# Performance work log

Hardware: AMD Instinct MI355X
Metric: run time of the kernel (lower is better)

The kernel has to match this reference:

```python
import math
import jax, jax.numpy as jnp
import numpy as np

B, N_COLS, CHANNELS, NUM_HEADS = 512, 128, 512, 8
D_HEAD = CHANNELS // NUM_HEADS


def setup_inputs() -> dict:
    key = jax.random.key(0)
    ks = jax.random.split(key, 9)
    s = 1.0 / math.sqrt(CHANNELS)
    x = jax.random.normal(ks[0], (B, N_COLS, CHANNELS), dtype=jnp.float32)
    Wq = jax.random.uniform(ks[1], (CHANNELS, CHANNELS), jnp.float32, -s, s)
    bq = jax.random.uniform(ks[2], (CHANNELS,), jnp.float32, -s, s)
    Wk = jax.random.uniform(ks[3], (CHANNELS, CHANNELS), jnp.float32, -s, s)
    bk = jax.random.uniform(ks[4], (CHANNELS,), jnp.float32, -s, s)
    Wv = jax.random.uniform(ks[5], (CHANNELS, CHANNELS), jnp.float32, -s, s)
    bv = jax.random.uniform(ks[6], (CHANNELS,), jnp.float32, -s, s)
    Wo = jax.random.uniform(ks[7], (CHANNELS, CHANNELS), jnp.float32, -s, s)
    bo = jax.random.uniform(ks[8], (CHANNELS,), jnp.float32, -s, s)
    return {"x": x, "Wq": Wq, "bq": bq, "Wk": Wk, "bk": bk,
            "Wv": Wv, "bv": bv, "Wo": Wo, "bo": bo}


def reference(x, Wq, bq, Wk, bk, Wv, bv, Wo, bo):
    b, n, c = x.shape
    h, d = NUM_HEADS, D_HEAD

    def split_heads(t):  # [b, n, c] -> [b, h, n, d]
        return t.reshape(b, n, h, d).transpose(0, 2, 1, 3)

    Q = split_heads(x @ Wq + bq)
    K = split_heads(x @ Wk + bk)
    V = split_heads(x @ Wv + bv)

    # raw scores [b, h, q, k]
    scores = jnp.einsum('bhqd,bhkd->bhqk', Q, K)
    # causal mask over columns; note: mask added BEFORE scaling by sqrt(d)
    causal = jnp.tril(jnp.ones((n, n), dtype=jnp.float32))
    mask = (1.0 - causal) * -100000.0
    attn = jax.nn.softmax((scores + mask) / math.sqrt(d), axis=-1)
    out = jnp.einsum('bhqk,bhkd->bhqd', attn, V)
    out = out.transpose(0, 2, 1, 3).reshape(b, n, c)
    return out @ Wo + bo
```

## Files before the change

kernel.cpp:

```cpp
#include <hip/hip_runtime.h>

typedef _Float16 f16;
typedef _Float16 half8 __attribute__((ext_vector_type(8)));
typedef _Float16 half4 __attribute__((ext_vector_type(4)));
typedef float f32x4 __attribute__((ext_vector_type(4)));

#define B_SZ 512
#define NQ   128
#define CH   512
#define NH   8
#define DH   64
#define MTOK (B_SZ*NQ)
#define KD   512

#define MFMA16(a,b,c) __builtin_amdgcn_mfma_f32_16x16x32_f16((a),(b),(c),0,0,0)

#define GLDS16(g,l) __builtin_amdgcn_global_load_lds( \
    (__attribute__((address_space(1))) void*)(g), \
    (__attribute__((address_space(3))) void*)(l), 16, 0, 0)

__global__ __launch_bounds__(256) void k_prep(
    const float* __restrict__ x,
    const float* __restrict__ Wq, const float* __restrict__ Wk,
    const float* __restrict__ Wv, const float* __restrict__ Wo,
    f16* __restrict__ xb, f16* __restrict__ wt) {
  const int bid = blockIdx.x;
  if (bid < 512) {
    for (int e = threadIdx.x; e < 2048; e += 256) {
      const int n = bid * 4 + (e >> 9);
      const int k = e & 511;
      const float* W = (n < 512) ? Wq : (n < 1024) ? Wk : (n < 1536) ? Wv : Wo;
      wt[n * 512 + k] = (f16)W[k * 512 + (n & 511)];
    }
  } else {
    const int n8 = MTOK * KD / 8;
    int i = (bid - 512) * 256 + threadIdx.x;
    const int stride = 2048 * 256;
    for (; i < n8; i += stride) {
      f32x4 a = ((const f32x4*)x)[2 * i];
      f32x4 b = ((const f32x4*)x)[2 * i + 1];
      half8 h;
      h[0] = (f16)a[0]; h[1] = (f16)a[1]; h[2] = (f16)a[2]; h[3] = (f16)a[3];
      h[4] = (f16)b[0]; h[5] = (f16)b[1]; h[6] = (f16)b[2]; h[7] = (f16)b[3];
      ((half8*)xb)[i] = h;
    }
  }
}

__device__ __forceinline__ void gemm128_bk64(
    const f16* __restrict__ gA,
    const f16* __restrict__ gB,
    f16* la, f16* lb, f32x4 (&acc)[4][4]) {
  const int tid = threadIdx.x;
  const int w = tid >> 6, lane = tid & 63;
  const int ln = lane & 15, g = lane >> 4;
  const int wr = w >> 1, wc = w & 1;

  const int ldst = w * 512;
  const int roA0 = (wr * 64 + ln) * 64;
  const int roB0 = (wc * 64 + ln) * 64;
  const int sx0 = ((0 * 4 + g) ^ (ln & 7)) * 8;
  const int sx1 = ((1 * 4 + g) ^ (ln & 7)) * 8;

#pragma unroll 1
  for (int kt = 0; kt < 8; ++kt) {
    const int k0 = kt * 64;
#pragma unroll
    for (int i = 0; i < 4; ++i) {
      GLDS16(gA + i * 32 * KD + k0, la + i * 2048 + ldst);
      GLDS16(gB + i * 32 * KD + k0, lb + i * 2048 + ldst);
    }
    __syncthreads();
    half8 af[4], bf[4];
#pragma unroll
    for (int ks = 0; ks < 2; ++ks) {
      const int sx = ks ? sx1 : sx0;
#pragma unroll
      for (int m = 0; m < 4; ++m)
        af[m] = *(const half8*)(la + roA0 + m * 1024 + sx);
#pragma unroll
      for (int n = 0; n < 4; ++n)
        bf[n] = *(const half8*)(lb + roB0 + n * 1024 + sx);
      __builtin_amdgcn_s_setprio(1);
#pragma unroll
      for (int m = 0; m < 4; ++m)
#pragma unroll
        for (int n = 0; n < 4; ++n)
          acc[m][n] = MFMA16(af[m], bf[n], acc[m][n]);
      __builtin_amdgcn_s_setprio(0);
    }
    __syncthreads();
  }
}

__device__ __forceinline__ int stage_src_off() {
  const int lane = threadIdx.x & 63, w = threadIdx.x >> 6;
  return (w * 8 + (lane >> 3)) * KD + (((lane & 7) ^ (lane >> 3)) << 3);
}

__global__ __launch_bounds__(256, 4) void k_qkv(
    const f16* __restrict__ A, const f16* __restrict__ Bw,
    const float* __restrict__ bq, const float* __restrict__ bk,
    const float* __restrict__ bv,
    f16* __restrict__ qb, f16* __restrict__ kb, f16* __restrict__ vb) {
  __shared__ f16 la[128 * 64];
  __shared__ f16 lb[128 * 64];
  const int tid = threadIdx.x;
  const int w = tid >> 6, lane = tid & 63;
  const int ln = lane & 15, g = lane >> 4;
  const int wr = w >> 1, wc = w & 1;
  const int s = blockIdx.x >> 3;
  const int ml = s / 12;
  const int ntile = s - ml * 12;
  const int mtile = (blockIdx.x & 7) * 64 + ml;

  const int so = stage_src_off();
  const f16* gA = A + mtile * 128 * KD + so;
  const f16* gB = Bw + ntile * 128 * KD + so;

  f32x4 acc[4][4] = {};
  gemm128_bk64(gA, gB, la, lb, acc);

  const int b = mtile;
  const int colbase = ntile * 128 + wc * 64;
#pragma unroll
  for (int m = 0; m < 4; ++m) {
    const int nn0 = wr * 64 + m * 16 + g * 4;
#pragma unroll
    for (int n = 0; n < 4; ++n) {
      const int col = colbase + n * 16 + ln;
      const int which = col >> 9;
      const int c = col & 511;
      const int h = c >> 6, d = c & 63;
      const float bias = (which == 0) ? bq[c] : (which == 1) ? bk[c] : bv[c];
      if (which < 2) {
        f16* dst = ((which == 0) ? qb : kb) + ((b * NH + h) * NQ + nn0) * DH + d;
#pragma unroll
        for (int r = 0; r < 4; ++r)
          dst[r * DH] = (f16)(acc[m][n][r] + bias);
      } else {
        half4 v4;
#pragma unroll
        for (int r = 0; r < 4; ++r)
          v4[r] = (f16)(acc[m][n][r] + bias);
        *(half4*)(vb + ((b * NH + h) * DH + d) * NQ + nn0) = v4;
      }
    }
  }
}

__global__ __launch_bounds__(256, 2) void k_attn(
    const f16* __restrict__ qbuf, const f16* __restrict__ kbuf,
    const f16* __restrict__ vbuf, f16* __restrict__ ao) {
  __shared__ f16 kl[128 * 72];
  __shared__ f16 vl[64 * 136];
  __shared__ f16 pl[128 * 136];
  const int bh = blockIdx.x;
  const f16* Qp = qbuf + bh * (NQ * DH);
  const f16* Kp = kbuf + bh * (NQ * DH);
  const f16* Vp = vbuf + bh * (DH * NQ);
  const int tid = threadIdx.x;
  const int w = tid >> 6, lane = tid & 63;
  const int ln = lane & 15, g = lane >> 4;

#pragma unroll
  for (int i = 0; i < 4; ++i) {
    const int e = i * 2048 + tid * 8;
    *(half8*)(kl + (e >> 6) * 72 + (e & 63)) = *(const half8*)(Kp + e);
  }
#pragma unroll
  for (int i = 0; i < 4; ++i) {
    const int e = i * 2048 + tid * 8;
    *(half8*)(vl + (e >> 7) * 136 + (e & 127)) = *(const half8*)(Vp + e);
  }
  half8 qf[2][2];
#pragma unroll
  for (int m = 0; m < 2; ++m)
#pragma unroll
    for (int ks = 0; ks < 2; ++ks)
      qf[m][ks] = *(const half8*)(Qp + (w * 32 + m * 16 + ln) * DH + ks * 32 + g * 8);
  __syncthreads();

  f32x4 s[2][8] = {};
#pragma unroll
  for (int ks = 0; ks < 2; ++ks)
#pragma unroll
    for (int n = 0; n < 8; ++n) {
      half8 kf = *(const half8*)(kl + (n * 16 + ln) * 72 + ks * 32 + g * 8);
      s[0][n] = MFMA16(qf[0][ks], kf, s[0][n]);
      s[1][n] = MFMA16(qf[1][ks], kf, s[1][n]);
    }

  float inv[2][4];
#pragma unroll
  for (int m = 0; m < 2; ++m) {
#pragma unroll
    for (int r = 0; r < 4; ++r) {
      const int q = w * 32 + m * 16 + g * 4 + r;
      float z[8];
      float rm = -1e30f;
#pragma unroll
      for (int n = 0; n < 8; ++n) {
        const int col = n * 16 + ln;
        float zz = s[m][n][r] * 0.125f + ((col > q) ? -12500.0f : 0.0f);
        z[n] = zz;
        rm = fmaxf(rm, zz);
      }
      rm = fmaxf(rm, __shfl_xor(rm, 1));
      rm = fmaxf(rm, __shfl_xor(rm, 2));
      rm = fmaxf(rm, __shfl_xor(rm, 4));
      rm = fmaxf(rm, __shfl_xor(rm, 8));
      float rs = 0.f;
#pragma unroll
      for (int n = 0; n < 8; ++n) {
        const float p = __expf(z[n] - rm);
        rs += p;
        pl[q * 136 + n * 16 + ln] = (f16)p;
      }
      rs += __shfl_xor(rs, 1);
      rs += __shfl_xor(rs, 2);
      rs += __shfl_xor(rs, 4);
      rs += __shfl_xor(rs, 8);
      inv[m][r] = 1.0f / rs;
    }
  }

  f32x4 o[2][4] = {};
#pragma unroll
  for (int ks = 0; ks < 4; ++ks) {
    half8 pf0 = *(const half8*)(pl + (w * 32 + ln) * 136 + ks * 32 + g * 8);
    half8 pf1 = *(const half8*)(pl + (w * 32 + 16 + ln) * 136 + ks * 32 + g * 8);
#pragma unroll
    for (int n = 0; n < 4; ++n) {
      half8 vf = *(const half8*)(vl + (n * 16 + ln) * 136 + ks * 32 + g * 8);
      o[0][n] = MFMA16(pf0, vf, o[0][n]);
      o[1][n] = MFMA16(pf1, vf, o[1][n]);
    }
  }

  __syncthreads();
#pragma unroll
  for (int m = 0; m < 2; ++m)
#pragma unroll
    for (int n = 0; n < 4; ++n)
#pragma unroll
      for (int r = 0; r < 4; ++r)
        pl[(w * 32 + m * 16 + g * 4 + r) * 136 + n * 16 + ln] =
            (f16)(o[m][n][r] * inv[m][r]);
  __syncthreads();
  const int b = bh >> 3, h = bh & 7;
  f16* dst = ao + (size_t)(b * NQ) * CH + h * DH;
  const int lr = lane >> 3, lc = lane & 7;
#pragma unroll
  for (int p = 0; p < 4; ++p) {
    const int q = w * 32 + p * 8 + lr;
    half8 v = *(const half8*)(pl + q * 136 + lc * 8);
    *(half8*)(dst + (size_t)q * CH + lc * 8) = v;
  }
}

__global__ __launch_bounds__(256, 4) void k_out(
    const f16* __restrict__ A, const f16* __restrict__ Bw,
    const float* __restrict__ bo, float* __restrict__ out) {
  __shared__ f16 la[128 * 64];
  __shared__ f16 lb[128 * 64];
  const int tid = threadIdx.x;
  const int w = tid >> 6, lane = tid & 63;
  const int ln = lane & 15, g = lane >> 4;
  const int wr = w >> 1, wc = w & 1;
  const int s = blockIdx.x >> 3;
  const int ml = s >> 2;
  const int ntile = s & 3;
  const int mtile = (blockIdx.x & 7) * 64 + ml;

  const int so = stage_src_off();
  const f16* gA = A + mtile * 128 * KD + so;
  const f16* gB = Bw + ntile * 128 * KD + so;

  f32x4 acc[4][4] = {};
  gemm128_bk64(gA, gB, la, lb, acc);

  const int colbase = ntile * 128 + wc * 64;
#pragma unroll
  for (int m = 0; m < 4; ++m) {
    const int tok0 = mtile * 128 + wr * 64 + m * 16 + g * 4;
#pragma unroll
    for (int n = 0; n < 4; ++n) {
      const int col = colbase + n * 16 + ln;
      const float bias = bo[col];
      float* dst = out + (size_t)tok0 * CH + col;
#pragma unroll
      for (int r = 0; r < 4; ++r)
        dst[r * CH] = acc[m][n][r] + bias;
    }
  }
}

extern "C" void kernel_launch(void* const* d_in, const int* in_sizes, int n_in,
                              void* d_out, int out_size, void* d_ws, size_t ws_size,
                              hipStream_t stream) {
  (void)in_sizes; (void)n_in; (void)out_size; (void)ws_size;
  const float* x  = (const float*)d_in[0];
  const float* Wq = (const float*)d_in[1];
  const float* bq = (const float*)d_in[2];
  const float* Wk = (const float*)d_in[3];
  const float* bk = (const float*)d_in[4];
  const float* Wv = (const float*)d_in[5];
  const float* bv = (const float*)d_in[6];
  const float* Wo = (const float*)d_in[7];
  const float* bo = (const float*)d_in[8];
  float* out = (float*)d_out;

  char* ws = (char*)d_ws;
  const size_t SZ = (size_t)MTOK * KD * sizeof(f16);
  f16* xb = (f16*)(ws);
  f16* qb = (f16*)(ws + SZ);
  f16* kb = (f16*)(ws + 2 * SZ);
  f16* vb = (f16*)(ws + 3 * SZ);
  f16* wt = (f16*)(ws + 4 * SZ);
  f16* ao = xb;

  k_prep<<<2560, 256, 0, stream>>>(x, Wq, Wk, Wv, Wo, xb, wt);
  k_qkv<<<6144, 256, 0, stream>>>(xb, wt, bq, bk, bv, qb, kb, vb);
  k_attn<<<4096, 256, 0, stream>>>(qb, kb, vb, ao);
  k_out<<<2048, 256, 0, stream>>>(ao, wt + 1536 * KD, bo, out);
}
```

Before: 297.6 us.

## Fuse x fp32-to-fp16 conversion into QKV GEMM with register-prefetched A tiles

Removes the separate pass that converted x to fp16. The QKV GEMM now reads fp32 x directly into registers, converts it and writes it to LDS, and prefetches the next k-tile while computing the current one. This saves a full 64MB fp32 read plus a 32MB fp16 write and read round trip. The cost is that each x tile is read again by all 12 N-tiles in fp32 (twice the bytes of fp16), register pressure rises, and occupancy is lowered to 3.

After: 330.8 us. +11.2%, slower.

```diff
diff --git a/kernel.cpp b/kernel.cpp
--- a/kernel.cpp
+++ b/kernel.cpp
@@ -20,76 +20,15 @@
     (__attribute__((address_space(3))) void*)(l), 16, 0, 0)
 
 __global__ __launch_bounds__(256) void k_prep(
-    const float* __restrict__ x,
     const float* __restrict__ Wq, const float* __restrict__ Wk,
     const float* __restrict__ Wv, const float* __restrict__ Wo,
-    f16* __restrict__ xb, f16* __restrict__ wt) {
+    f16* __restrict__ wt) {
   const int bid = blockIdx.x;
-  if (bid < 512) {
-    for (int e = threadIdx.x; e < 2048; e += 256) {
-      const int n = bid * 4 + (e >> 9);
-      const int k = e & 511;
-      const float* W = (n < 512) ? Wq : (n < 1024) ? Wk : (n < 1536) ? Wv : Wo;
-      wt[n * 512 + k] = (f16)W[k * 512 + (n & 511)];
-    }
-  } else {
-    const int n8 = MTOK * KD / 8;
-    int i = (bid - 512) * 256 + threadIdx.x;
-    const int stride = 2048 * 256;
-    for (; i < n8; i += stride) {
-      f32x4 a = ((const f32x4*)x)[2 * i];
-      f32x4 b = ((const f32x4*)x)[2 * i + 1];
-      half8 h;
-      h[0] = (f16)a[0]; h[1] = (f16)a[1]; h[2] = (f16)a[2]; h[3] = (f16)a[3];
-      h[4] = (f16)b[0]; h[5] = (f16)b[1]; h[6] = (f16)b[2]; h[7] = (f16)b[3];
-      ((half8*)xb)[i] = h;
-    }
-  }
-}
-
-__device__ __forceinline__ void gemm128_bk64(
-    const f16* __restrict__ gA,
-    const f16* __restrict__ gB,
-    f16* la, f16* lb, f32x4 (&acc)[4][4]) {
-  const int tid = threadIdx.x;
-  const int w = tid >> 6, lane = tid & 63;
-  const int ln = lane & 15, g = lane >> 4;
-  const int wr = w >> 1, wc = w & 1;
-
-  const int ldst = w * 512;
-  const int roA0 = (wr * 64 + ln) * 64;
-  const int roB0 = (wc * 64 + ln) * 64;
-  const int sx0 = ((0 * 4 + g) ^ (ln & 7)) * 8;
-  const int sx1 = ((1 * 4 + g) ^ (ln & 7)) * 8;
-
-#pragma unroll 1
-  for (int kt = 0; kt < 8; ++kt) {
-    const int k0 = kt * 64;
-#pragma unroll
-    for (int i = 0; i < 4; ++i) {
-      GLDS16(gA + i * 32 * KD + k0, la + i * 2048 + ldst);
-      GLDS16(gB + i * 32 * KD + k0, lb + i * 2048 + ldst);
-    }
-    __syncthreads();
-    half8 af[4], bf[4];
-#pragma unroll
-    for (int ks = 0; ks < 2; ++ks) {
-      const int sx = ks ? sx1 : sx0;
-#pragma unroll
-      for (int m = 0; m < 4; ++m)
-        af[m] = *(const half8*)(la + roA0 + m * 1024 + sx);
-#pragma unroll
-      for (int n = 0; n < 4; ++n)
-        bf[n] = *(const half8*)(lb + roB0 + n * 1024 + sx);
-      __builtin_amdgcn_s_setprio(1);
-#pragma unroll
-      for (int m = 0; m < 4; ++m)
-#pragma unroll
-        for (int n = 0; n < 4; ++n)
-          acc[m][n] = MFMA16(af[m], bf[n], acc[m][n]);
-      __builtin_amdgcn_s_setprio(0);
-    }
-    __syncthreads();
+  for (int e = threadIdx.x; e < 2048; e += 256) {
+    const int n = bid * 4 + (e >> 9);
+    const int k = e & 511;
+    const float* W = (n < 512) ? Wq : (n < 1024) ? Wk : (n < 1536) ? Wv : Wo;
+    wt[n * 512 + k] = (f16)W[k * 512 + (n & 511)];
   }
 }
 
@@ -98,8 +37,22 @@
   return (w * 8 + (lane >> 3)) * KD + (((lane & 7) ^ (lane >> 3)) << 3);
 }
 
-__global__ __launch_bounds__(256, 4) void k_qkv(
-    const f16* __restrict__ A, const f16* __restrict__ Bw,
+#define CMP_BODY(la, lb) do { \
+  half8 af[4], bf[4]; \
+  _Pragma("unroll") for (int ks = 0; ks < 2; ++ks) { \
+    const int sx = ks ? sx1 : sx0; \
+    _Pragma("unroll") for (int m = 0; m < 4; ++m) \
+      af[m] = *(const half8*)((la) + roA0 + m * 1024 + sx); \
+    _Pragma("unroll") for (int n = 0; n < 4; ++n) \
+      bf[n] = *(const half8*)((lb) + roB0 + n * 1024 + sx); \
+    __builtin_amdgcn_s_setprio(1); \
+    _Pragma("unroll") for (int m = 0; m < 4; ++m) \
+      _Pragma("unroll") for (int n = 0; n < 4; ++n) \
+        acc[m][n] = MFMA16(af[m], bf[n], acc[m][n]); \
+    __builtin_amdgcn_s_setprio(0); } } while (0)
+
+__global__ __launch_bounds__(256, 3) void k_qkv(
+    const float* __restrict__ x, const f16* __restrict__ Bw,
     const float* __restrict__ bq, const float* __restrict__ bk,
     const float* __restrict__ bv,
     f16* __restrict__ qb, f16* __restrict__ kb, f16* __restrict__ vb) {
@@ -114,12 +67,55 @@
   const int ntile = s - ml * 12;
   const int mtile = (blockIdx.x & 7) * 64 + ml;
 
-  const int so = stage_src_off();
-  const f16* gA = A + mtile * 128 * KD + so;
-  const f16* gB = Bw + ntile * 128 * KD + so;
+  const int w512 = w * 512;
+  const int roA0 = (wr * 64 + ln) * 64;
+  const int roB0 = (wc * 64 + ln) * 64;
+  const int sx0 = ((0 + g) ^ (ln & 7)) * 8;
+  const int sx1 = ((4 + g) ^ (ln & 7)) * 8;
+
+  const float* gAx = x + (size_t)(mtile * 128 + w * 8 + (lane >> 3)) * KD +
+                     (((lane & 7) ^ (lane >> 3)) << 3);
+  const f16* gBs = Bw + ntile * 128 * KD + stage_src_off();
+
+  f32x4 ar[4][2];
+#define ALOAD(K0) do { _Pragma("unroll") \
+  for (int i = 0; i < 4; ++i) { \
+    ar[i][0] = *(const f32x4*)(gAx + i * 32 * KD + (K0)); \
+    ar[i][1] = *(const f32x4*)(gAx + i * 32 * KD + (K0) + 4); } } while (0)
+#define AWRITE() do { _Pragma("unroll") \
+  for (int i = 0; i < 4; ++i) { \
+    half8 h; \
+    _Pragma("unroll") for (int j = 0; j < 4; ++j) { \
+      h[j] = (f16)ar[i][0][j]; h[4 + j] = (f16)ar[i][1][j]; } \
+    *(half8*)(la + i * 2048 + w512 + lane * 8) = h; } } while (0)
+#define BSTAGE(K0) do { _Pragma("unroll") \
+  for (int i = 0; i < 4; ++i) \
+    GLDS16(gBs + i * 32 * KD + (K0), lb + i * 2048 + w512); } while (0)
 
   f32x4 acc[4][4] = {};
-  gemm128_bk64(gA, gB, la, lb, acc);
+  ALOAD(0);
+
+#pragma unroll 1
+  for (int t = 0; t < 7; ++t) {
+    const int k0 = t * 64;
+    BSTAGE(k0);
+    asm volatile("s_waitcnt vmcnt(4)" ::: "memory");
+    AWRITE();
+    ALOAD(k0 + 64);
+    asm volatile("s_waitcnt vmcnt(8) lgkmcnt(0)" ::: "memory");
+    __builtin_amdgcn_s_barrier();
+    CMP_BODY(la, lb);
+    __builtin_amdgcn_s_barrier();
+  }
+  BSTAGE(448);
+  asm volatile("s_waitcnt vmcnt(4)" ::: "memory");
+  AWRITE();
+  asm volatile("s_waitcnt vmcnt(0) lgkmcnt(0)" ::: "memory");
+  __builtin_amdgcn_s_barrier();
+  CMP_BODY(la, lb);
+#undef ALOAD
+#undef AWRITE
+#undef BSTAGE
 
   const int b = mtile;
   const int colbase = ntile * 128 + wc * 64;
@@ -273,12 +269,29 @@
   const int ntile = s & 3;
   const int mtile = (blockIdx.x & 7) * 64 + ml;
 
+  const int w512 = w * 512;
+  const int roA0 = (wr * 64 + ln) * 64;
+  const int roB0 = (wc * 64 + ln) * 64;
+  const int sx0 = ((0 + g) ^ (ln & 7)) * 8;
+  const int sx1 = ((4 + g) ^ (ln & 7)) * 8;
+
   const int so = stage_src_off();
   const f16* gA = A + mtile * 128 * KD + so;
   const f16* gB = Bw + ntile * 128 * KD + so;
 
   f32x4 acc[4][4] = {};
-  gemm128_bk64(gA, gB, la, lb, acc);
+#pragma unroll 1
+  for (int kt = 0; kt < 8; ++kt) {
+    const int k0 = kt * 64;
+#pragma unroll
+    for (int i = 0; i < 4; ++i) {
+      GLDS16(gA + i * 32 * KD + k0, la + i * 2048 + w512);
+      GLDS16(gB + i * 32 * KD + k0, lb + i * 2048 + w512);
+    }
+    __syncthreads();
+    CMP_BODY(la, lb);
+    __syncthreads();
+  }
 
   const int colbase = ntile * 128 + wc * 64;
 #pragma unroll
@@ -313,15 +326,14 @@
 
   char* ws = (char*)d_ws;
   const size_t SZ = (size_t)MTOK * KD * sizeof(f16);
-  f16* xb = (f16*)(ws);
+  f16* ao = (f16*)(ws);
   f16* qb = (f16*)(ws + SZ);
   f16* kb = (f16*)(ws + 2 * SZ);
   f16* vb = (f16*)(ws + 3 * SZ);
   f16* wt = (f16*)(ws + 4 * SZ);
-  f16* ao = xb;
-
-  k_prep<<<2560, 256, 0, stream>>>(x, Wq, Wk, Wv, Wo, xb, wt);
-  k_qkv<<<6144, 256, 0, stream>>>(xb, wt, bq, bk, bv, qb, kb, vb);
+
+  k_prep<<<512, 256, 0, stream>>>(Wq, Wk, Wv, Wo, wt);
+  k_qkv<<<6144, 256, 0, stream>>>(x, wt, bq, bk, bv, qb, kb, vb);
   k_attn<<<4096, 256, 0, stream>>>(qb, kb, vb, ao);
   k_out<<<2048, 256, 0, stream>>>(ao, wt + 1536 * KD, bo, out);
 }
```

## Enlarge QKV and output GEMM tiles to 256x128 with 512-thread blocks

Applied to the files above, without the earlier changes.

The QKV projection and output projection GEMMs now use 256x128 tiles computed by 8 waves (512 threads) instead of 128x128 tiles with 4 waves. The B (weight) tile is shared across twice as many rows, which cuts weight loads and halves the block count. The staging offsets and swizzle are reworked for the larger block, and epilogue index math maps rows to two batch entries per tile. The larger shared-memory footprint (48KB) and 512-thread blocks may lower occupancy per CU.

Measured after the change: 313.5 us. 1.05x slower.

```diff
diff --git a/kernel.cpp b/kernel.cpp
--- a/kernel.cpp
+++ b/kernel.cpp
@@ -47,7 +47,12 @@
   }
 }
 
-__device__ __forceinline__ void gemm128_bk64(
+__device__ __forceinline__ int stage_src_off() {
+  const int tid = threadIdx.x;
+  return (tid >> 3) * KD + (((tid & 7) ^ ((tid >> 3) & 7)) << 3);
+}
+
+__device__ __forceinline__ void gemm256x128_bk64(
     const f16* __restrict__ gA,
     const f16* __restrict__ gB,
     f16* la, f16* lb, f32x4 (&acc)[4][4]) {
@@ -56,20 +61,21 @@
   const int ln = lane & 15, g = lane >> 4;
   const int wr = w >> 1, wc = w & 1;
 
-  const int ldst = w * 512;
+  const int w512 = w * 512;
   const int roA0 = (wr * 64 + ln) * 64;
   const int roB0 = (wc * 64 + ln) * 64;
-  const int sx0 = ((0 * 4 + g) ^ (ln & 7)) * 8;
-  const int sx1 = ((1 * 4 + g) ^ (ln & 7)) * 8;
+  const int sx0 = ((0 + g) ^ (ln & 7)) * 8;
+  const int sx1 = ((4 + g) ^ (ln & 7)) * 8;
 
 #pragma unroll 1
   for (int kt = 0; kt < 8; ++kt) {
     const int k0 = kt * 64;
 #pragma unroll
-    for (int i = 0; i < 4; ++i) {
-      GLDS16(gA + i * 32 * KD + k0, la + i * 2048 + ldst);
-      GLDS16(gB + i * 32 * KD + k0, lb + i * 2048 + ldst);
-    }
+    for (int i = 0; i < 4; ++i)
+      GLDS16(gA + i * 64 * KD + k0, la + i * 4096 + w512);
+#pragma unroll
+    for (int i = 0; i < 2; ++i)
+      GLDS16(gB + i * 64 * KD + k0, lb + i * 4096 + w512);
     __syncthreads();
     half8 af[4], bf[4];
 #pragma unroll
@@ -93,17 +99,12 @@
   }
 }
 
-__device__ __forceinline__ int stage_src_off() {
-  const int lane = threadIdx.x & 63, w = threadIdx.x >> 6;
-  return (w * 8 + (lane >> 3)) * KD + (((lane & 7) ^ (lane >> 3)) << 3);
-}
-
-__global__ __launch_bounds__(256, 4) void k_qkv(
+__global__ __launch_bounds__(512, 4) void k_qkv(
     const f16* __restrict__ A, const f16* __restrict__ Bw,
     const float* __restrict__ bq, const float* __restrict__ bk,
     const float* __restrict__ bv,
     f16* __restrict__ qb, f16* __restrict__ kb, f16* __restrict__ vb) {
-  __shared__ f16 la[128 * 64];
+  __shared__ f16 la[256 * 64];
   __shared__ f16 lb[128 * 64];
   const int tid = threadIdx.x;
   const int w = tid >> 6, lane = tid & 63;
@@ -112,20 +113,21 @@
   const int s = blockIdx.x >> 3;
   const int ml = s / 12;
   const int ntile = s - ml * 12;
-  const int mtile = (blockIdx.x & 7) * 64 + ml;
+  const int mtile = (blockIdx.x & 7) * 32 + ml;
 
   const int so = stage_src_off();
-  const f16* gA = A + mtile * 128 * KD + so;
+  const f16* gA = A + (size_t)mtile * 256 * KD + so;
   const f16* gB = Bw + ntile * 128 * KD + so;
 
   f32x4 acc[4][4] = {};
-  gemm128_bk64(gA, gB, la, lb, acc);
-
-  const int b = mtile;
+  gemm256x128_bk64(gA, gB, la, lb, acc);
+
   const int colbase = ntile * 128 + wc * 64;
 #pragma unroll
   for (int m = 0; m < 4; ++m) {
-    const int nn0 = wr * 64 + m * 16 + g * 4;
+    const int grow = wr * 64 + m * 16 + g * 4;
+    const int b = mtile * 2 + (grow >> 7);
+    const int nn0 = grow & 127;
 #pragma unroll
     for (int n = 0; n < 4; ++n) {
       const int col = colbase + n * 16 + ln;
@@ -259,10 +261,10 @@
   }
 }
 
-__global__ __launch_bounds__(256, 4) void k_out(
+__global__ __launch_bounds__(512, 4) void k_out(
     const f16* __restrict__ A, const f16* __restrict__ Bw,
     const float* __restrict__ bo, float* __restrict__ out) {
-  __shared__ f16 la[128 * 64];
+  __shared__ f16 la[256 * 64];
   __shared__ f16 lb[128 * 64];
   const int tid = threadIdx.x;
   const int w = tid >> 6, lane = tid & 63;
@@ -271,19 +273,19 @@
   const int s = blockIdx.x >> 3;
   const int ml = s >> 2;
   const int ntile = s & 3;
-  const int mtile = (blockIdx.x & 7) * 64 + ml;
+  const int mtile = (blockIdx.x & 7) * 32 + ml;
 
   const int so = stage_src_off();
-  const f16* gA = A + mtile * 128 * KD + so;
+  const f16* gA = A + (size_t)mtile * 256 * KD + so;
   const f16* gB = Bw + ntile * 128 * KD + so;
 
   f32x4 acc[4][4] = {};
-  gemm128_bk64(gA, gB, la, lb, acc);
+  gemm256x128_bk64(gA, gB, la, lb, acc);
 
   const int colbase = ntile * 128 + wc * 64;
 #pragma unroll
   for (int m = 0; m < 4; ++m) {
-    const int tok0 = mtile * 128 + wr * 64 + m * 16 + g * 4;
+    const int tok0 = mtile * 256 + wr * 64 + m * 16 + g * 4;
 #pragma unroll
     for (int n = 0; n < 4; ++n) {
       const int col = colbase + n * 16 + ln;
@@ -321,7 +323,7 @@
   f16* ao = xb;
 
   k_prep<<<2560, 256, 0, stream>>>(x, Wq, Wk, Wv, Wo, xb, wt);
-  k_qkv<<<6144, 256, 0, stream>>>(xb, wt, bq, bk, bv, qb, kb, vb);
+  k_qkv<<<3072, 512, 0, stream>>>(xb, wt, bq, bk, bv, qb, kb, vb);
   k_attn<<<4096, 256, 0, stream>>>(qb, kb, vb, ao);
-  k_out<<<2048, 256, 0, stream>>>(ao, wt + 1536 * KD, bo, out);
-}
+  k_out<<<1024, 512, 0, stream>>>(ao, wt + 1536 * KD, bo, out);
+}
```
